# Kernel optimization log

Hardware: AMD Instinct MI355X
Metric: run time of the kernel (lower is better)

## Reference

```python
import jax, jax.numpy as jnp
import numpy as np

B, CIN, COUT = 8, 8, 8
NX, NT = 512, 512
M1, M2 = 4, 4


def setup_inputs() -> dict:
    key = jax.random.key(0)
    k1, k2, k3 = jax.random.split(key, 3)
    scale = 1.0 / (CIN * COUT)
    x = jax.random.normal(k1, (B, CIN, NX, NT), dtype=jnp.float32)
    T = jnp.arange(NT, dtype=jnp.float32).reshape(1, NT)  # time grid
    X = jnp.arange(NX, dtype=jnp.float32).reshape(1, NX)  # space grid
    weights1_ri = scale * jax.random.uniform(k2, (CIN, COUT, M1, M2, 2), dtype=jnp.float32)
    weights2_ri = scale * jax.random.uniform(k3, (CIN, COUT, M1, M2, 2), dtype=jnp.float32)
    return {"x": x, "T": T, "X": X, "weights1_ri": weights1_ri, "weights2_ri": weights2_ri}


def reference(x, T, X, weights1_ri, weights2_ri):
    # subsample every other grid point (as in the torch forward)
    xs = x[:, :, ::2, ::2]                      # [B, Cin, Hs, Ws]
    tx = T[:, ::2]                              # [1, Ws]
    ty = X[:, ::2]                              # [1, Hs]
    dty = ty[0, 1] - ty[0, 0]
    dtx = tx[0, 1] - tx[0, 0]
    Hs, Ws = xs.shape[-2], xs.shape[-1]
    Wr = Ws // 2 + 1

    FW1 = jnp.fft.rfft2(xs)                     # [B, Cin, Hs, Wr] complex64

    two_pi_i = 2.0 * jnp.pi * 1j
    lam1 = (jnp.fft.fftfreq(Hs).astype(jnp.float32) / dty).astype(jnp.complex64) * two_pi_i   # [Hs]
    lam2 = (jnp.fft.rfftfreq(Ws).astype(jnp.float32) / dtx).astype(jnp.complex64) * two_pi_i  # [Wr]

    w1 = (weights1_ri[..., 0] + 1j * weights1_ri[..., 1]).astype(jnp.complex64)
    w2 = (weights2_ri[..., 0] + 1j * weights2_ri[..., 1]).astype(jnp.complex64)

    out2 = jnp.zeros((xs.shape[0], w1.shape[1], Hs, Wr), dtype=jnp.complex64)
    out2 = out2.at[:, :, :M1, :M2].set(
        jnp.einsum('bixy,ioxy->boxy', FW1[:, :, :M1, :M2], w1))
    out2 = out2.at[:, :, -M1:, :M2].set(
        jnp.einsum('bixy,ioxy->boxy', FW1[:, :, -M1:, :M2], w2))

    # inverse transform onto the FULL (non-subsampled) grid via complex exponentials.
    # Same math as the original rank-4 term6 einsum, factorized separably.
    E1 = jnp.exp(lam1[:, None] * X.astype(jnp.complex64).reshape(1, -1))  # [Hs, NX]
    E2 = jnp.exp(lam2[:, None] * T.astype(jnp.complex64).reshape(1, -1))  # [Wr, NT]

    tmp = jnp.einsum('boxw,xz->bozw', out2, E1)   # [B, Cout, NX, Wr]
    x2 = jnp.einsum('bozw,wi->bozi', tmp, E2)     # [B, Cout, NX, NT]
    return jnp.real(x2) / (Ws * Hs)
```

## Files before the change

### kernel.cpp

```cpp
#include <hip/hip_runtime.h>
#include <hip/hip_bf16.h>


#define PI2 6.283185307179586f

typedef float vfloat4 __attribute__((ext_vector_type(4)));

__device__ __forceinline__ float foldred(float u, float v, int msk, int lane) {
    float send = (lane & msk) ? u : v;
    float recv = __shfl_xor(send, msk, 64);
    return ((lane & msk) ? v : u) + recv;
}

__device__ __forceinline__ float fold8(const float* ar, const float* ai, int lane) {
    float A0 = foldred(ar[0], ai[0], 1, lane);
    float A1 = foldred(ar[1], ai[1], 1, lane);
    float A2 = foldred(ar[2], ai[2], 1, lane);
    float A3 = foldred(ar[3], ai[3], 1, lane);
    float B0 = foldred(A0, A1, 2, lane);
    float B1 = foldred(A2, A3, 2, lane);
    float C  = foldred(B0, B1, 4, lane);
    C += __shfl_xor(C, 8, 64);
    C += __shfl_xor(C, 16, 64);
    C += __shfl_xor(C, 32, 64);
    return C;
}

__global__ __launch_bounds__(256) void k_dft_t(const float* __restrict__ x,
                                               float* __restrict__ Yg) {
    __shared__ float vals[4][64];
    int lane = threadIdx.x & 63;
    int w    = threadIdx.x >> 6;
    int bc   = blockIdx.x >> 4;
    int g    = blockIdx.x & 15;
    int y0   = g * 16 + w * 4;

    const float* base = x + (size_t)bc * 512 * 512;

    vfloat4 A0[4], A1[4];
#pragma unroll
    for (int r = 0; r < 4; ++r) {
        const vfloat4* row = (const vfloat4*)(base + (size_t)(2 * (y0 + r)) * 512);
        A0[r] = __builtin_nontemporal_load(&row[lane]);
        A1[r] = __builtin_nontemporal_load(&row[lane + 64]);
    }

    float s, c;
    sincosf((PI2 / 128.0f) * (float)lane, &s, &c);
    float er[4], ei[4], orE[4], oiE[4];
    er[0] = 1.f; ei[0] = 0.f;
    er[1] = c;   ei[1] = -s;
    er[2] = er[1]*er[1] - ei[1]*ei[1];  ei[2] = 2.f*er[1]*ei[1];
    er[3] = er[2]*er[1] - ei[2]*ei[1];  ei[3] = er[2]*ei[1] + ei[2]*er[1];
    const float rr1 = 0.999698818696204f, ri1 = -0.024541228522912f;
    const float rr2 = 0.998795456205172f, ri2 = -0.049067674327418f;
    const float rr3 = 0.997290456678690f, ri3 = -0.073564563599667f;
    orE[0] = 1.f; oiE[0] = 0.f;
    orE[1] = er[1]*rr1 - ei[1]*ri1;  oiE[1] = er[1]*ri1 + ei[1]*rr1;
    orE[2] = er[2]*rr2 - ei[2]*ri2;  oiE[2] = er[2]*ri2 + ei[2]*rr2;
    orE[3] = er[3]*rr3 - ei[3]*ri3;  oiE[3] = er[3]*ri3 + ei[3]*rr3;

    int midx = lane >> 3;
    float mf = (midx < 4) ? (float)midx : (float)(midx - 8);
    float snm, csm;
    sincosf((PI2 / 256.0f) * mf * (float)y0, &snm, &csm);
    float cs = csm, ty = -snm;
    float smm, cmm;
    sincosf((PI2 / 256.0f) * mf, &smm, &cmm);

    float acc = 0.f;
#pragma unroll
    for (int r = 0; r < 4; ++r) {
        float s0 = A0[r][0] + A1[r][0], d0 = A0[r][0] - A1[r][0];
        float s2 = A0[r][2] + A1[r][2], d2 = A0[r][2] - A1[r][2];
        float ar[4], ai[4];
#pragma unroll
        for (int kw = 0; kw < 4; ++kw) {
            float E = (kw & 1) ? d0 : s0;
            float O = (kw & 1) ? d2 : s2;
            ar[kw] = E * er[kw] + O * orE[kw];
            ai[kw] = E * ei[kw] + O * oiE[kw];
        }
        float C  = fold8(ar, ai, lane);
        float pt = __shfl_xor(C, 1, 64);
        float sel = (lane & 1) ? ty : -ty;
        acc += C * cs + pt * sel;
        float nc = cs * cmm + ty * smm;
        float nt = ty * cmm - cs * smm;
        cs = nc; ty = nt;
    }
    vals[w][lane] = acc;
    __syncthreads();

    if (threadIdx.x < 64) {
        int b = bc >> 3, ci = bc & 7;
        float sum = vals[0][lane] + vals[1][lane] + vals[2][lane] + vals[3][lane];
        Yg[((size_t)((b * 16 + g) * 8 + ci)) * 64 + lane] = sum;
    }
}

__global__ __launch_bounds__(256) void k_mix_eval(const float* __restrict__ Yg,
                                                  const float* __restrict__ w1,
                                                  const float* __restrict__ w2,
                                                  float* __restrict__ out) {
    __shared__ float vals[4][64];
    __shared__ float lcf[64];

    int lane  = threadIdx.x & 63;
    int w     = threadIdx.x >> 6;
    int bo    = blockIdx.x >> 5;
    int chunk = blockIdx.x & 31;
    int b = bo >> 3, o = bo & 7;

    {
        int midx = lane >> 3, kw = (lane >> 1) & 3, ri = lane & 1, mx = midx & 3;
        const float* wt = (midx < 4) ? w1 : w2;
        float wr_[8], swi_[8];
#pragma unroll
        for (int ci = 0; ci < 8; ++ci) {
            const float* wp = wt + ((((ci * 8 + o) * 4 + mx) * 4 + kw) * 2);
            wr_[ci]  = wp[0];
            swi_[ci] = ri ? wp[1] : -wp[1];
        }
        float acc = 0.f;
#pragma unroll
        for (int gi = 0; gi < 4; ++gi) {
            int g = w + gi * 4;
            const float* Yp = Yg + ((size_t)((b * 16 + g) * 8)) * 64 + lane;
#pragma unroll
            for (int ci = 0; ci < 8; ++ci) {
                float Yv = Yp[ci * 64];
                float pt = __shfl_xor(Yv, 1, 64);
                acc += Yv * wr_[ci] + pt * swi_[ci];
            }
        }
        vals[w][lane] = acc;
    }
    __syncthreads();
    if (w == 0)
        lcf[lane] = vals[0][lane] + vals[1][lane] + vals[2][lane] + vals[3][lane];
    __syncthreads();

    float c1b, s1b;
    sincosf((PI2 / 512.0f) * (float)(lane * 4), &s1b, &c1b);
    const float cr = 0.99992470183839f;
    const float sr = 0.012271538285720f;
    const float inv = 1.0f / 65536.0f;

    int ll = lane & 31;
    int kw = ll & 3, midx = (ll >> 2) & 7;
    float m = (midx < 4) ? (float)midx : (float)(midx - 8);
    float2 cc = make_float2(lcf[ll * 2], lcf[ll * 2 + 1]);
    float sgm = (midx & 1) ? -1.f : 1.f;

#pragma unroll
    for (int e = 0; e < 2; ++e) {
        int z = chunk * 8 + w * 2 + e;

        float ang = (PI2 / 512.0f) * m * (float)z;
        float s, c;
        sincosf(ang, &s, &c);
        float hx = cc.x * c - cc.y * s;
        float hy = cc.x * s + cc.y * c;
        float gx = sgm * hx, gy = sgm * hy;

        float F = foldred(hx, hy, 4, lane);
        F += __shfl_xor(F, 8, 64);
        F += __shfl_xor(F, 16, 64);
        float G = foldred(gx, gy, 4, lane);
        G += __shfl_xor(G, 8, 64);
        G += __shfl_xor(G, 16, 64);
        float h0x = __shfl(F, 0, 64);
        float h1x = __shfl(F, 1, 64), h2x = __shfl(F, 2, 64), h3x = __shfl(F, 3, 64);
        float h1y = __shfl(F, 5, 64), h2y = __shfl(F, 6, 64), h3y = __shfl(F, 7, 64);
        float g0x = __shfl(G, 0, 64);
        float g1x = __shfl(G, 1, 64), g2x = __shfl(G, 2, 64), g3x = __shfl(G, 3, 64);
        float g1y = __shfl(G, 5, 64), g2y = __shfl(G, 6, 64), g3y = __shfl(G, 7, 64);

        float* orow0 = out + (size_t)(bo * 512 + z) * 512;
        float* orow1 = orow0 + 256 * 512;

        float c1 = c1b, s1 = s1b;
        vfloat4 r0, r1, q0, q1;
#pragma unroll
        for (int j = 0; j < 4; ++j) {
            float c2a = c1 * c1 - s1 * s1, s2a = 2.f * c1 * s1;
            float c3a = c2a * c1 - s2a * s1, s3a = s2a * c1 + c2a * s1;
            float t1 = h1x * c1  - h1y * s1;
            float t2 = h2x * c2a - h2y * s2a;
            float t3 = h3x * c3a - h3y * s3a;
            r0[j] = (h0x + t1 + t2 + t3) * inv;
            r1[j] = (h0x - t1 + t2 - t3) * inv;
            float u1 = g1x * c1  - g1y * s1;
            float u2 = g2x * c2a - g2y * s2a;
            float u3 = g3x * c3a - g3y * s3a;
            q0[j] = (g0x + u1 + u2 + u3) * inv;
            q1[j] = (g0x - u1 + u2 - u3) * inv;
            float nc = c1 * cr - s1 * sr;
            float ns = s1 * cr + c1 * sr;
            c1 = nc; s1 = ns;
        }
        __builtin_nontemporal_store(r0, (vfloat4*)(orow0 + lane * 4));
        __builtin_nontemporal_store(r1, (vfloat4*)(orow0 + 256 + lane * 4));
        __builtin_nontemporal_store(q0, (vfloat4*)(orow1 + lane * 4));
        __builtin_nontemporal_store(q1, (vfloat4*)(orow1 + 256 + lane * 4));
    }
}

extern "C" void kernel_launch(void* const* d_in, const int* in_sizes, int n_in,
                              void* d_out, int out_size, void* d_ws, size_t ws_size,
                              hipStream_t stream) {
    const float* x  = (const float*)d_in[0];
    const float* w1 = (const float*)d_in[3];
    const float* w2 = (const float*)d_in[4];
    float* out = (float*)d_out;

    float* Yg = (float*)d_ws;

    k_dft_t<<<1024, 256, 0, stream>>>(x, Yg);
    k_mix_eval<<<2048, 256, 0, stream>>>(Yg, w1, w2, out);
}
```

Measured before the change: 25.62 us.

## Fuse DFT and mix/eval kernels into one persistent-style kernel with per-batch spin barrier

Merges the forward partial-DFT stage and the mode-mixing/evaluation stage into a single kernel of 2048 blocks. Each block first computes a two-row partial DFT, publishes it with release atomics and bumps a per-batch counter, then spins until all 256 producer blocks for its batch are done before mixing and writing output. The aim is to remove the second launch and the inter-kernel gap, while keeping the old two-kernel path as a fallback when occupancy is too low for all blocks to be resident. The cost is an extra memset launch, spin-wait barriers that deadlock if not all blocks are co-resident, and twice as many partial sums to reduce in the mix stage.

```diff
diff --git a/kernel.cpp b/kernel.cpp
--- a/kernel.cpp
+++ b/kernel.cpp
@@ -26,91 +26,97 @@
     return C;
 }
 
-__global__ __launch_bounds__(256) void k_dft_t(const float* __restrict__ x,
-                                               float* __restrict__ Yg) {
-    __shared__ float vals[4][64];
-    int lane = threadIdx.x & 63;
-    int w    = threadIdx.x >> 6;
-    int bc   = blockIdx.x >> 4;
-    int g    = blockIdx.x & 15;
-    int y0   = g * 16 + w * 4;
-
-    const float* base = x + (size_t)bc * 512 * 512;
-
-    vfloat4 A0[4], A1[4];
-#pragma unroll
-    for (int r = 0; r < 4; ++r) {
-        const vfloat4* row = (const vfloat4*)(base + (size_t)(2 * (y0 + r)) * 512);
-        A0[r] = __builtin_nontemporal_load(&row[lane]);
-        A1[r] = __builtin_nontemporal_load(&row[lane + 64]);
-    }
-
-    float s, c;
-    sincosf((PI2 / 128.0f) * (float)lane, &s, &c);
-    float er[4], ei[4], orE[4], oiE[4];
-    er[0] = 1.f; ei[0] = 0.f;
-    er[1] = c;   ei[1] = -s;
-    er[2] = er[1]*er[1] - ei[1]*ei[1];  ei[2] = 2.f*er[1]*ei[1];
-    er[3] = er[2]*er[1] - ei[2]*ei[1];  ei[3] = er[2]*ei[1] + ei[2]*er[1];
-    const float rr1 = 0.999698818696204f, ri1 = -0.024541228522912f;
-    const float rr2 = 0.998795456205172f, ri2 = -0.049067674327418f;
-    const float rr3 = 0.997290456678690f, ri3 = -0.073564563599667f;
-    orE[0] = 1.f; oiE[0] = 0.f;
-    orE[1] = er[1]*rr1 - ei[1]*ri1;  oiE[1] = er[1]*ri1 + ei[1]*rr1;
-    orE[2] = er[2]*rr2 - ei[2]*ri2;  oiE[2] = er[2]*ri2 + ei[2]*rr2;
-    orE[3] = er[3]*rr3 - ei[3]*ri3;  oiE[3] = er[3]*ri3 + ei[3]*rr3;
-
-    int midx = lane >> 3;
-    float mf = (midx < 4) ? (float)midx : (float)(midx - 8);
-    float snm, csm;
-    sincosf((PI2 / 256.0f) * mf * (float)y0, &snm, &csm);
-    float cs = csm, ty = -snm;
-    float smm, cmm;
-    sincosf((PI2 / 256.0f) * mf, &smm, &cmm);
-
-    float acc = 0.f;
-#pragma unroll
-    for (int r = 0; r < 4; ++r) {
-        float s0 = A0[r][0] + A1[r][0], d0 = A0[r][0] - A1[r][0];
-        float s2 = A0[r][2] + A1[r][2], d2 = A0[r][2] - A1[r][2];
-        float ar[4], ai[4];
-#pragma unroll
-        for (int kw = 0; kw < 4; ++kw) {
-            float E = (kw & 1) ? d0 : s0;
-            float O = (kw & 1) ? d2 : s2;
-            ar[kw] = E * er[kw] + O * orE[kw];
-            ai[kw] = E * ei[kw] + O * oiE[kw];
-        }
-        float C  = fold8(ar, ai, lane);
-        float pt = __shfl_xor(C, 1, 64);
-        float sel = (lane & 1) ? ty : -ty;
-        acc += C * cs + pt * sel;
-        float nc = cs * cmm + ty * smm;
-        float nt = ty * cmm - cs * smm;
-        cs = nc; ty = nt;
-    }
-    vals[w][lane] = acc;
-    __syncthreads();
-
-    if (threadIdx.x < 64) {
-        int b = bc >> 3, ci = bc & 7;
-        float sum = vals[0][lane] + vals[1][lane] + vals[2][lane] + vals[3][lane];
-        Yg[((size_t)((b * 16 + g) * 8 + ci)) * 64 + lane] = sum;
-    }
-}
-
-__global__ __launch_bounds__(256) void k_mix_eval(const float* __restrict__ Yg,
+__global__ __launch_bounds__(256, 8) void k_fused(const float* __restrict__ x,
                                                   const float* __restrict__ w1,
                                                   const float* __restrict__ w2,
+                                                  float* __restrict__ Yg,
+                                                  unsigned int* __restrict__ done,
                                                   float* __restrict__ out) {
     __shared__ float vals[4][64];
     __shared__ float lcf[64];
 
-    int lane  = threadIdx.x & 63;
-    int w     = threadIdx.x >> 6;
-    int bo    = blockIdx.x >> 5;
-    int chunk = blockIdx.x & 31;
-    int b = bo >> 3, o = bo & 7;
+    int lane = threadIdx.x & 63;
+    int w    = threadIdx.x >> 6;
+    int b    = blockIdx.x & 7;
+    int t    = blockIdx.x >> 3;
+
+    {
+        int ci = t >> 5, g = t & 31;
+        int bc = b * 8 + ci;
+        int y0 = g * 8 + w * 2;
+
+        const vfloat4* r0 = (const vfloat4*)(x + ((size_t)bc * 512 + (size_t)(2 * y0)) * 512);
+        const vfloat4* r1 = (const vfloat4*)(x + ((size_t)bc * 512 + (size_t)(2 * y0 + 2)) * 512);
+        vfloat4 a0 = __builtin_nontemporal_load(&r0[lane]);
+        vfloat4 a1 = __builtin_nontemporal_load(&r0[lane + 64]);
+        vfloat4 b0 = __builtin_nontemporal_load(&r1[lane]);
+        vfloat4 b1 = __builtin_nontemporal_load(&r1[lane + 64]);
+
+        float s, c;
+        sincosf((PI2 / 128.0f) * (float)lane, &s, &c);
+        float er[4], ei[4], orE[4], oiE[4];
+        er[0] = 1.f; ei[0] = 0.f;
+        er[1] = c;   ei[1] = -s;
+        er[2] = er[1]*er[1] - ei[1]*ei[1];  ei[2] = 2.f*er[1]*ei[1];
+        er[3] = er[2]*er[1] - ei[2]*ei[1];  ei[3] = er[2]*ei[1] + ei[2]*er[1];
+        const float rr1 = 0.999698818696204f, ri1 = -0.024541228522912f;
+        const float rr2 = 0.998795456205172f, ri2 = -0.049067674327418f;
+        const float rr3 = 0.997290456678690f, ri3 = -0.073564563599667f;
+        orE[0] = 1.f; oiE[0] = 0.f;
+        orE[1] = er[1]*rr1 - ei[1]*ri1;  oiE[1] = er[1]*ri1 + ei[1]*rr1;
+        orE[2] = er[2]*rr2 - ei[2]*ri2;  oiE[2] = er[2]*ri2 + ei[2]*rr2;
+        orE[3] = er[3]*rr3 - ei[3]*ri3;  oiE[3] = er[3]*ri3 + ei[3]*rr3;
+
+        float arA[4], aiA[4], arB[4], aiB[4];
+#pragma unroll
+        for (int kw = 0; kw < 4; ++kw) {
+            float sgn = (kw & 1) ? -1.f : 1.f;
+            float eA = a0[0] + sgn * a1[0], oA = a0[2] + sgn * a1[2];
+            float eB = b0[0] + sgn * b1[0], oB = b0[2] + sgn * b1[2];
+            arA[kw] = eA * er[kw] + oA * orE[kw];
+            aiA[kw] = eA * ei[kw] + oA * oiE[kw];
+            arB[kw] = eB * er[kw] + oB * orE[kw];
+            aiB[kw] = eB * ei[kw] + oB * oiE[kw];
+        }
+        float Ca = fold8(arA, aiA, lane);
+        float Cb = fold8(arB, aiB, lane);
+
+        int midx = lane >> 3;
+        float mf = (midx < 4) ? (float)midx : (float)(midx - 8);
+        float snm, csm;
+        sincosf((PI2 / 256.0f) * mf * (float)y0, &snm, &csm);
+        float ty0 = -snm;
+        float smm, cmm;
+        sincosf((PI2 / 256.0f) * mf, &smm, &cmm);
+        float cs1 = csm * cmm + ty0 * smm;
+        float ty1 = ty0 * cmm - csm * smm;
+
+        float pa = __shfl_xor(Ca, 1, 64);
+        float pb = __shfl_xor(Cb, 1, 64);
+        float selA = (lane & 1) ? ty0 : -ty0;
+        float selB = (lane & 1) ? ty1 : -ty1;
+        vals[w][lane] = Ca * csm + pa * selA + Cb * cs1 + pb * selB;
+        __syncthreads();
+
+        if (threadIdx.x < 64) {
+            float sum = vals[0][lane] + vals[1][lane] + vals[2][lane] + vals[3][lane];
+            __hip_atomic_store(&Yg[((size_t)((b * 32 + g) * 8 + ci)) * 64 + lane], sum,
+                               __ATOMIC_RELEASE, __HIP_MEMORY_SCOPE_AGENT);
+        }
+        __syncthreads();
+        if (threadIdx.x == 0)
+            __hip_atomic_fetch_add(&done[b], 1u, __ATOMIC_RELEASE, __HIP_MEMORY_SCOPE_AGENT);
+    }
+
+    if (threadIdx.x == 0) {
+        while (__hip_atomic_load(&done[b], __ATOMIC_ACQUIRE, __HIP_MEMORY_SCOPE_AGENT) < 256u)
+            __builtin_amdgcn_s_sleep(2);
+    }
+    __syncthreads();
+
+    int o     = t >> 5;
+    int chunk = t & 31;
+    int bo    = b * 8 + o;
 
     {
         int midx = lane >> 3, kw = (lane >> 1) & 3, ri = lane & 1, mx = midx & 3;
@@ -124,12 +130,13 @@
         }
         float acc = 0.f;
 #pragma unroll
-        for (int gi = 0; gi < 4; ++gi) {
+        for (int gi = 0; gi < 8; ++gi) {
             int g = w + gi * 4;
-            const float* Yp = Yg + ((size_t)((b * 16 + g) * 8)) * 64 + lane;
+            float* Yp = Yg + ((size_t)((b * 32 + g) * 8)) * 64 + lane;
 #pragma unroll
             for (int ci = 0; ci < 8; ++ci) {
-                float Yv = Yp[ci * 64];
+                float Yv = __hip_atomic_load(Yp + ci * 64, __ATOMIC_RELAXED,
+                                             __HIP_MEMORY_SCOPE_AGENT);
                 float pt = __shfl_xor(Yv, 1, 64);
                 acc += Yv * wr_[ci] + pt * swi_[ci];
             }
@@ -150,7 +157,7 @@
     int ll = lane & 31;
     int kw = ll & 3, midx = (ll >> 2) & 7;
     float m = (midx < 4) ? (float)midx : (float)(midx - 8);
-    float2 cc = make_float2(lcf[ll * 2], lcf[ll * 2 + 1]);
+    float2 cc = make_float2(lcf[(midx * 4 + kw) * 2], lcf[(midx * 4 + kw) * 2 + 1]);
     float sgm = (midx & 1) ? -1.f : 1.f;
 
 #pragma unroll
@@ -207,6 +214,176 @@
     }
 }
 
+__global__ __launch_bounds__(256) void k_dft_t(const float* __restrict__ x,
+                                               float* __restrict__ Yg) {
+    __shared__ float vals[4][64];
+    int lane = threadIdx.x & 63;
+    int w    = threadIdx.x >> 6;
+    int bc   = blockIdx.x >> 4;
+    int g    = blockIdx.x & 15;
+    int y0   = g * 16 + w * 4;
+
+    const float* base = x + (size_t)bc * 512 * 512;
+    vfloat4 A0[4], A1[4];
+#pragma unroll
+    for (int r = 0; r < 4; ++r) {
+        const vfloat4* row = (const vfloat4*)(base + (size_t)(2 * (y0 + r)) * 512);
+        A0[r] = __builtin_nontemporal_load(&row[lane]);
+        A1[r] = __builtin_nontemporal_load(&row[lane + 64]);
+    }
+    float s, c;
+    sincosf((PI2 / 128.0f) * (float)lane, &s, &c);
+    float er[4], ei[4], orE[4], oiE[4];
+    er[0] = 1.f; ei[0] = 0.f;
+    er[1] = c;   ei[1] = -s;
+    er[2] = er[1]*er[1] - ei[1]*ei[1];  ei[2] = 2.f*er[1]*ei[1];
+    er[3] = er[2]*er[1] - ei[2]*ei[1];  ei[3] = er[2]*ei[1] + ei[2]*er[1];
+    const float rr1 = 0.999698818696204f, ri1 = -0.024541228522912f;
+    const float rr2 = 0.998795456205172f, ri2 = -0.049067674327418f;
+    const float rr3 = 0.997290456678690f, ri3 = -0.073564563599667f;
+    orE[0] = 1.f; oiE[0] = 0.f;
+    orE[1] = er[1]*rr1 - ei[1]*ri1;  oiE[1] = er[1]*ri1 + ei[1]*rr1;
+    orE[2] = er[2]*rr2 - ei[2]*ri2;  oiE[2] = er[2]*ri2 + ei[2]*rr2;
+    orE[3] = er[3]*rr3 - ei[3]*ri3;  oiE[3] = er[3]*ri3 + ei[3]*rr3;
+
+    int midx = lane >> 3;
+    float mf = (midx < 4) ? (float)midx : (float)(midx - 8);
+    float snm, csm;
+    sincosf((PI2 / 256.0f) * mf * (float)y0, &snm, &csm);
+    float cs = csm, ty = -snm;
+    float smm, cmm;
+    sincosf((PI2 / 256.0f) * mf, &smm, &cmm);
+
+    float acc = 0.f;
+#pragma unroll
+    for (int r = 0; r < 4; ++r) {
+        float s0 = A0[r][0] + A1[r][0], d0 = A0[r][0] - A1[r][0];
+        float s2 = A0[r][2] + A1[r][2], d2 = A0[r][2] - A1[r][2];
+        float ar[4], ai[4];
+#pragma unroll
+        for (int kw = 0; kw < 4; ++kw) {
+            float E = (kw & 1) ? d0 : s0;
+            float O = (kw & 1) ? d2 : s2;
+            ar[kw] = E * er[kw] + O * orE[kw];
+            ai[kw] = E * ei[kw] + O * oiE[kw];
+        }
+        float C  = fold8(ar, ai, lane);
+        float pt = __shfl_xor(C, 1, 64);
+        float sel = (lane & 1) ? ty : -ty;
+        acc += C * cs + pt * sel;
+        float nc = cs * cmm + ty * smm;
+        float nt = ty * cmm - cs * smm;
+        cs = nc; ty = nt;
+    }
+    vals[w][lane] = acc;
+    __syncthreads();
+    if (threadIdx.x < 64) {
+        int b = bc >> 3, ci = bc & 7;
+        float sum = vals[0][lane] + vals[1][lane] + vals[2][lane] + vals[3][lane];
+        Yg[((size_t)((b * 16 + g) * 8 + ci)) * 64 + lane] = sum;
+    }
+}
+
+__global__ __launch_bounds__(256) void k_mix_eval(const float* __restrict__ Yg,
+                                                  const float* __restrict__ w1,
+                                                  const float* __restrict__ w2,
+                                                  float* __restrict__ out) {
+    __shared__ float vals[4][64];
+    __shared__ float lcf[64];
+    int lane  = threadIdx.x & 63;
+    int w     = threadIdx.x >> 6;
+    int bo    = blockIdx.x >> 5;
+    int chunk = blockIdx.x & 31;
+    int b = bo >> 3, o = bo & 7;
+    {
+        int midx = lane >> 3, kw = (lane >> 1) & 3, ri = lane & 1, mx = midx & 3;
+        const float* wt = (midx < 4) ? w1 : w2;
+        float wr_[8], swi_[8];
+#pragma unroll
+        for (int ci = 0; ci < 8; ++ci) {
+            const float* wp = wt + ((((ci * 8 + o) * 4 + mx) * 4 + kw) * 2);
+            wr_[ci]  = wp[0];
+            swi_[ci] = ri ? wp[1] : -wp[1];
+        }
+        float acc = 0.f;
+#pragma unroll
+        for (int gi = 0; gi < 4; ++gi) {
+            int g = w + gi * 4;
+            const float* Yp = Yg + ((size_t)((b * 16 + g) * 8)) * 64 + lane;
+#pragma unroll
+            for (int ci = 0; ci < 8; ++ci) {
+                float Yv = Yp[ci * 64];
+                float pt = __shfl_xor(Yv, 1, 64);
+                acc += Yv * wr_[ci] + pt * swi_[ci];
+            }
+        }
+        vals[w][lane] = acc;
+    }
+    __syncthreads();
+    if (w == 0)
+        lcf[lane] = vals[0][lane] + vals[1][lane] + vals[2][lane] + vals[3][lane];
+    __syncthreads();
+
+    float c1b, s1b;
+    sincosf((PI2 / 512.0f) * (float)(lane * 4), &s1b, &c1b);
+    const float cr = 0.99992470183839f;
+    const float sr = 0.012271538285720f;
+    const float inv = 1.0f / 65536.0f;
+    int ll = lane & 31;
+    int kw = ll & 3, midx = (ll >> 2) & 7;
+    float m = (midx < 4) ? (float)midx : (float)(midx - 8);
+    float2 cc = make_float2(lcf[ll * 2], lcf[ll * 2 + 1]);
+    float sgm = (midx & 1) ? -1.f : 1.f;
+#pragma unroll
+    for (int e = 0; e < 2; ++e) {
+        int z = chunk * 8 + w * 2 + e;
+        float ang = (PI2 / 512.0f) * m * (float)z;
+        float s, c;
+        sincosf(ang, &s, &c);
+        float hx = cc.x * c - cc.y * s;
+        float hy = cc.x * s + cc.y * c;
+        float gx = sgm * hx, gy = sgm * hy;
+        float F = foldred(hx, hy, 4, lane);
+        F += __shfl_xor(F, 8, 64);
+        F += __shfl_xor(F, 16, 64);
+        float G = foldred(gx, gy, 4, lane);
+        G += __shfl_xor(G, 8, 64);
+        G += __shfl_xor(G, 16, 64);
+        float h0x = __shfl(F, 0, 64);
+        float h1x = __shfl(F, 1, 64), h2x = __shfl(F, 2, 64), h3x = __shfl(F, 3, 64);
+        float h1y = __shfl(F, 5, 64), h2y = __shfl(F, 6, 64), h3y = __shfl(F, 7, 64);
+        float g0x = __shfl(G, 0, 64);
+        float g1x = __shfl(G, 1, 64), g2x = __shfl(G, 2, 64), g3x = __shfl(G, 3, 64);
+        float g1y = __shfl(G, 5, 64), g2y = __shfl(G, 6, 64), g3y = __shfl(G, 7, 64);
+        float* orow0 = out + (size_t)(bo * 512 + z) * 512;
+        float* orow1 = orow0 + 256 * 512;
+        float c1 = c1b, s1 = s1b;
+        vfloat4 r0, r1, q0, q1;
+#pragma unroll
+        for (int j = 0; j < 4; ++j) {
+            float c2a = c1 * c1 - s1 * s1, s2a = 2.f * c1 * s1;
+            float c3a = c2a * c1 - s2a * s1, s3a = s2a * c1 + c2a * s1;
+            float t1 = h1x * c1  - h1y * s1;
+            float t2 = h2x * c2a - h2y * s2a;
+            float t3 = h3x * c3a - h3y * s3a;
+            r0[j] = (h0x + t1 + t2 + t3) * inv;
+            r1[j] = (h0x - t1 + t2 - t3) * inv;
+            float u1 = g1x * c1  - g1y * s1;
+            float u2 = g2x * c2a - g2y * s2a;
+            float u3 = g3x * c3a - g3y * s3a;
+            q0[j] = (g0x + u1 + u2 + u3) * inv;
+            q1[j] = (g0x - u1 + u2 - u3) * inv;
+            float nc = c1 * cr - s1 * sr;
+            float ns = s1 * cr + c1 * sr;
+            c1 = nc; s1 = ns;
+        }
+        __builtin_nontemporal_store(r0, (vfloat4*)(orow0 + lane * 4));
+        __builtin_nontemporal_store(r1, (vfloat4*)(orow0 + 256 + lane * 4));
+        __builtin_nontemporal_store(q0, (vfloat4*)(orow1 + lane * 4));
+        __builtin_nontemporal_store(q1, (vfloat4*)(orow1 + 256 + lane * 4));
+    }
+}
+
 extern "C" void kernel_launch(void* const* d_in, const int* in_sizes, int n_in,
                               void* d_out, int out_size, void* d_ws, size_t ws_size,
                               hipStream_t stream) {
@@ -216,7 +393,18 @@
     float* out = (float*)d_out;
 
     float* Yg = (float*)d_ws;
-
-    k_dft_t<<<1024, 256, 0, stream>>>(x, Yg);
-    k_mix_eval<<<2048, 256, 0, stream>>>(Yg, w1, w2, out);
-}
+    unsigned int* done = (unsigned int*)(Yg + 131072);
+
+    int maxb = 0;
+    bool fused_ok =
+        (hipOccupancyMaxActiveBlocksPerMultiprocessor(&maxb, (const void*)k_fused, 256, 0)
+             == hipSuccess) && (maxb >= 8);
+
+    if (fused_ok) {
+        hipMemsetAsync(done, 0, 8 * sizeof(unsigned int), stream);
+        k_fused<<<2048, 256, 0, stream>>>(x, w1, w2, Yg, done, out);
+    } else {
+        k_dft_t<<<1024, 256, 0, stream>>>(x, Yg);
+        k_mix_eval<<<2048, 256, 0, stream>>>(Yg, w1, w2, out);
+    }
+}
```

After: 25.71 us. About the same (+0.4%).
